# Optimization experiments

Hardware: AMD Instinct MI355X
Metric: run time of the kernel (lower is better)

## Reference

```python
import jax, jax.numpy as jnp
import numpy as np


def _gcn_conv(x, src, dst, W, b, n):
    """PyG-style GCNConv: symmetric-normalized aggregation with self-loops.
    out = D^{-1/2} (A + I) D^{-1/2} X W + b, deg computed with self-loops.
    """
    xw = x @ W  # [n, out]
    ones = jnp.ones(src.shape[0], dtype=x.dtype)
    deg = jax.ops.segment_sum(ones, dst, num_segments=n) + 1.0  # +1 self-loop
    dinv = jax.lax.rsqrt(deg)
    coef = dinv[src] * dinv[dst]  # [E]
    msg = xw[src] * coef[:, None]  # [E, out] gather + scale
    agg = jax.ops.segment_sum(msg, dst, num_segments=n)
    agg = agg + xw * (dinv * dinv)[:, None]  # self-loop term, norm = 1/deg
    return agg + b


def setup_inputs() -> dict:
    key = jax.random.key(0)
    ks = jax.random.split(key, 7)
    N, E = 500000, 8000000
    x = jax.random.normal(ks[0], (N, 2), dtype=jnp.float32)
    y1 = jax.random.normal(ks[1], (N,), dtype=jnp.float32)
    edge_index = jax.random.randint(ks[2], (2, E), 0, N, dtype=jnp.int64)
    s = 0.2
    W1 = jax.random.normal(ks[3], (3, 29), dtype=jnp.float32) * s
    b1 = jnp.zeros((29,), dtype=jnp.float32)
    W2 = jax.random.normal(ks[4], (32, 29), dtype=jnp.float32) * s
    b2 = jnp.zeros((29,), dtype=jnp.float32)
    W3 = jax.random.normal(ks[5], (32, 1), dtype=jnp.float32) * s
    b3 = jnp.zeros((1,), dtype=jnp.float32)
    return {"x": x, "y1": y1, "edge_index": edge_index,
            "W1": W1, "b1": b1, "W2": W2, "b2": b2, "W3": W3, "b3": b3}


def reference(x, y1, edge_index, W1, b1, W2, b2, W3, b3):
    n = x.shape[0]
    src, dst = edge_index[0], edge_index[1]
    inp = jnp.concatenate([x, y1[:, None]], axis=1)  # [N, 3]
    h = jax.nn.relu(_gcn_conv(inp, src, dst, W1, b1, n))  # [N, 29]
    h = jnp.concatenate([h, inp], axis=1)  # [N, 32] skip
    h = jax.nn.relu(_gcn_conv(h, src, dst, W2, b2, n))  # [N, 29]
    h = jnp.concatenate([h, inp], axis=1)  # [N, 32] skip
    h = _gcn_conv(h, src, dst, W3, b3, n)  # [N, 1]
    return h.reshape(-1)
```

## Files before the change

kernel.cpp:

```cpp
#include <hip/hip_runtime.h>
#include <hip/hip_fp16.h>


#define CAPB       17920
#define BSH2       10
#define BN2        1024
#define PACK_SHIFT 19
#define PACK_MASK  0x7FFFFu
#define SPLIT_CH   8192
#define DEST_CAP   17408

typedef int v4i __attribute__((ext_vector_type(4)));

__global__ __launch_bounds__(512) void split_kernel(
    const int* __restrict__ src, const int* __restrict__ dst,
    unsigned int* __restrict__ gcur, unsigned int* __restrict__ ebuf, int E) {
    __shared__ unsigned int hist[512];
    __shared__ unsigned int delta[512];
    __shared__ unsigned int wsum[8];
    __shared__ unsigned int tots;
    __shared__ unsigned int staged[SPLIT_CH];
    __shared__ unsigned short bid[SPLIT_CH];
    int tid = threadIdx.x;
    long long base = (long long)blockIdx.x * SPLIT_CH;
    hist[tid] = 0;
    __syncthreads();
    unsigned int s[16], d[16];
    if (base + SPLIT_CH <= E) {
        const v4i* s4 = (const v4i*)(src + base);
        const v4i* d4 = (const v4i*)(dst + base);
#pragma unroll
        for (int i = 0; i < 4; i++) {
            v4i sv = __builtin_nontemporal_load(s4 + tid + 512 * i);
            v4i dv = __builtin_nontemporal_load(d4 + tid + 512 * i);
            s[4 * i + 0] = (unsigned int)sv.x; d[4 * i + 0] = (unsigned int)dv.x;
            s[4 * i + 1] = (unsigned int)sv.y; d[4 * i + 1] = (unsigned int)dv.y;
            s[4 * i + 2] = (unsigned int)sv.z; d[4 * i + 2] = (unsigned int)dv.z;
            s[4 * i + 3] = (unsigned int)sv.w; d[4 * i + 3] = (unsigned int)dv.w;
        }
#pragma unroll
        for (int i = 0; i < 16; i++) atomicAdd(&hist[d[i] >> BSH2], 1u);
    } else {
#pragma unroll
        for (int i = 0; i < 16; i++) {
            long long e = base + tid + 512 * i;
            bool ok = e < E;
            s[i] = ok ? (unsigned int)src[e] : 0u;
            d[i] = ok ? (unsigned int)dst[e] : 0xFFFFFFFFu;
            if (ok) atomicAdd(&hist[d[i] >> BSH2], 1u);
        }
    }
    __syncthreads();
    unsigned int c = hist[tid];
    unsigned int v = c;
#pragma unroll
    for (int off = 1; off < 64; off <<= 1) {
        unsigned int t = __shfl_up(v, off, 64);
        if ((tid & 63) >= off) v += t;
    }
    int wv = tid >> 6;
    if ((tid & 63) == 63) wsum[wv] = v;
    __syncthreads();
    if (tid == 0) {
        unsigned int r = 0;
#pragma unroll
        for (int i = 0; i < 8; i++) { unsigned int t = wsum[i]; wsum[i] = r; r += t; }
        tots = r;
    }
    __syncthreads();
    unsigned int excl = v + wsum[wv] - c;
    unsigned int gb = c ? atomicAdd(&gcur[tid], c) : 0u;
    delta[tid] = gb - excl;
    hist[tid] = excl;
    __syncthreads();
#pragma unroll
    for (int i = 0; i < 16; i++) {
        if (d[i] != 0xFFFFFFFFu) {
            unsigned int bb = d[i] >> BSH2;
            unsigned int pos = atomicAdd(&hist[bb], 1u);
            staged[pos] = s[i] | ((d[i] & (BN2 - 1)) << PACK_SHIFT);
            bid[pos] = (unsigned short)bb;
        }
    }
    __syncthreads();
    unsigned int tot = tots;
    for (unsigned int i = tid; i < tot; i += 512) {
        unsigned int bb = bid[i];
        unsigned int rel = delta[bb] + i;
        if (rel < CAPB) ebuf[(size_t)bb * CAPB + rel] = staged[i];
    }
}

__global__ __launch_bounds__(1024) void build1_kernel(
    const unsigned int* __restrict__ gcur, const unsigned int* __restrict__ ebuf,
    const float* __restrict__ x, const float* __restrict__ y1,
    unsigned int* __restrict__ rowdeg, float4* __restrict__ u0,
    uint2* __restrict__ u0h, int N) {
    __shared__ unsigned int hist[BN2];
    __shared__ unsigned int wsum[16];
    int b = blockIdx.x, tid = threadIdx.x;
    hist[tid] = 0;
    unsigned int T = gcur[b]; if (T > CAPB) T = CAPB;
    const unsigned int* seg = ebuf + (size_t)b * CAPB;
    __syncthreads();
    for (unsigned int f = tid; f < T; f += 1024)
        atomicAdd(&hist[seg[f] >> PACK_SHIFT], 1u);
    __syncthreads();
    unsigned int cnt = hist[tid];
    unsigned int v = cnt;
#pragma unroll
    for (int off = 1; off < 64; off <<= 1) {
        unsigned int t = __shfl_up(v, off, 64);
        if ((tid & 63) >= off) v += t;
    }
    int wv = tid >> 6;
    if ((tid & 63) == 63) wsum[wv] = v;
    __syncthreads();
    if (tid == 0) {
        unsigned int r = 0;
#pragma unroll
        for (int i = 0; i < 16; i++) { unsigned int t = wsum[i]; wsum[i] = r; r += t; }
    }
    __syncthreads();
    unsigned int base = v + wsum[wv] - cnt;
    int n = (b << BSH2) + tid;
    if (n < N) {
        rowdeg[n] = base | (cnt << 16);
        float di = rsqrtf((float)cnt + 1.0f);
        float v0 = x[2 * n] * di, v1 = x[2 * n + 1] * di, v2 = y1[n] * di;
        u0[n] = make_float4(v0, v1, v2, di);
        union { __half2 h2[2]; uint2 u; } pk;
        pk.h2[0] = __floats2half2_rn(v0, v1);
        pk.h2[1] = __floats2half2_rn(v2, 0.f);
        u0h[n] = pk.u;
    }
}

__device__ __forceinline__ unsigned int sfetch2(const unsigned int* dest,
                                                const unsigned int* seg2,
                                                unsigned int j) {
    return (j < DEST_CAP) ? dest[j] : seg2[j];
}

__device__ __forceinline__ void walk_node(
    int gn, int q, unsigned int o, unsigned int e,
    const unsigned int* __restrict__ dest, const unsigned int* __restrict__ seg2,
    const uint2* __restrict__ u0h, const float4* __restrict__ u0,
    const float* __restrict__ W1, const float* __restrict__ b1,
    uint4* __restrict__ h1s) {
    unsigned int cnt = e - o;
    unsigned int hcnt = cnt >> 1;
    unsigned int j0 = o + (q ? hcnt : 0), j1 = q ? e : o + hcnt;
    float4 u = u0[gn];
    float sx = q ? 0.f : u.x, sy = q ? 0.f : u.y, sz = q ? 0.f : u.z;
    unsigned int j = j0;
    for (; j + 4 <= j1; j += 4) {
        unsigned int i0 = sfetch2(dest, seg2, j);
        unsigned int i1 = sfetch2(dest, seg2, j + 1);
        unsigned int i2 = sfetch2(dest, seg2, j + 2);
        unsigned int i3 = sfetch2(dest, seg2, j + 3);
        union { uint2 u; __half2 h[2]; } g0, g1, g2, g3;
        g0.u = u0h[i0]; g1.u = u0h[i1]; g2.u = u0h[i2]; g3.u = u0h[i3];
        float2 a0 = __half22float2(g0.h[0]), c0 = __half22float2(g0.h[1]);
        float2 a1 = __half22float2(g1.h[0]), c1 = __half22float2(g1.h[1]);
        float2 a2 = __half22float2(g2.h[0]), c2 = __half22float2(g2.h[1]);
        float2 a3 = __half22float2(g3.h[0]), c3 = __half22float2(g3.h[1]);
        sx += (a0.x + a1.x) + (a2.x + a3.x);
        sy += (a0.y + a1.y) + (a2.y + a3.y);
        sz += (c0.x + c1.x) + (c2.x + c3.x);
    }
    for (; j < j1; j++) {
        union { uint2 u; __half2 h[2]; } g;
        g.u = u0h[sfetch2(dest, seg2, j)];
        float2 a = __half22float2(g.h[0]);
        sx += a.x; sy += a.y; sz += __half2float(g.h[1].x);
    }
    sx += __shfl_xor(sx, 1, 64);
    sy += __shfl_xor(sy, 1, 64);
    sz += __shfl_xor(sz, 1, 64);
    float di = u.w;
    float a0 = sx * di, a1 = sy * di, a2 = sz * di;
    float hv[16];
#pragma unroll
    for (int i = 0; i < 16; i++) {
        int k = 16 * q + i;
        if (k < 29) {
            float vv = fmaf(a0, W1[k], fmaf(a1, W1[29 + k], fmaf(a2, W1[58 + k], b1[k])));
            hv[i] = fmaxf(vv, 0.0f) * di;
        } else {
            hv[i] = (k == 29) ? a0 : (k == 30) ? a1 : a2;
        }
    }
    union { __half2 h2[8]; uint4 u4[2]; } pk;
#pragma unroll
    for (int i = 0; i < 8; i++) pk.h2[i] = __floats2half2_rn(hv[2 * i], hv[2 * i + 1]);
    uint4* row = h1s + (size_t)gn * 4 + 2 * q;
    row[0] = pk.u4[0];
    row[1] = pk.u4[1];
}

__global__ __launch_bounds__(1024) void build2_kernel(
    const unsigned int* __restrict__ gcur, const unsigned int* __restrict__ ebuf,
    const unsigned int* __restrict__ rowdeg, const float4* __restrict__ u0,
    const uint2* __restrict__ u0h,
    const float* __restrict__ W1, const float* __restrict__ b1,
    unsigned int* __restrict__ ebuf2, uint4* __restrict__ h1s, int N) {
    __shared__ unsigned int cur[BN2];
    __shared__ unsigned int base2[BN2 + 1];
    __shared__ unsigned int dest[DEST_CAP];
    int b = blockIdx.x, tid = threadIdx.x;
    int gn0 = (b << BSH2);
    int n = gn0 + tid;
    unsigned int T = gcur[b]; if (T > CAPB) T = CAPB;
    unsigned int off = (n < N) ? (rowdeg[n] & 0xFFFFu) : T;
    cur[tid] = off; base2[tid] = off;
    if (tid == 0) base2[BN2] = T;
    const unsigned int* seg = ebuf + (size_t)b * CAPB;
    unsigned int* seg2 = ebuf2 + (size_t)b * CAPB;
    __syncthreads();
    for (unsigned int f = tid; f < T; f += 1024) {
        unsigned int p = seg[f];
        unsigned int dloc = p >> PACK_SHIFT;
        unsigned int pos = atomicAdd(&cur[dloc], 1u);
        unsigned int s = p & PACK_MASK;
        if (pos < DEST_CAP) dest[pos] = s;
        else                seg2[pos] = s;
    }
    __syncthreads();
    unsigned int m = T < DEST_CAP ? T : DEST_CAP;
    for (unsigned int i = tid; i < m; i += 1024) seg2[i] = dest[i];
    int q = tid & 1;
    int l0 = tid >> 1;
    int gnA = gn0 + l0;
    if (gnA < N)
        walk_node(gnA, q, base2[l0], base2[l0 + 1], dest, seg2, u0h, u0, W1, b1, h1s);
    int l1 = l0 + 512;
    int gnB = gn0 + l1;
    if (gnB < N)
        walk_node(gnB, q, base2[l1], base2[l1 + 1], dest, seg2, u0h, u0, W1, b1, h1s);
}

__device__ __forceinline__ void unpack8(float4 r, float* o) {
    union { float4 f; __half2 h[4]; } u; u.f = r;
    float2 a = __half22float2(u.h[0]); o[0] = a.x; o[1] = a.y;
    float2 b = __half22float2(u.h[1]); o[2] = b.x; o[3] = b.y;
    float2 c = __half22float2(u.h[2]); o[4] = c.x; o[5] = c.y;
    float2 d = __half22float2(u.h[3]); o[6] = d.x; o[7] = d.y;
}

__global__ __launch_bounds__(256) void pull2_kernel(
    const float4* __restrict__ h1f4, const unsigned int* __restrict__ rowdeg,
    const unsigned int* __restrict__ ebuf2, const float4* __restrict__ u0,
    const float* __restrict__ x, const float* __restrict__ y1,
    const float* __restrict__ W2, const float* __restrict__ b2,
    const float* __restrict__ W3, const float* __restrict__ b3,
    __half* __restrict__ zs, float* __restrict__ out, int N) {
    __shared__ float W2l[32 * 29];
    for (int i = threadIdx.x; i < 32 * 29; i += 256) W2l[i] = W2[i];
    int t = blockIdx.x * 256 + threadIdx.x;
    int n = t >> 2, q = t & 3;
    __syncthreads();
    if (n >= N) return;
    unsigned int rd = rowdeg[n];
    const unsigned int* lst = ebuf2 + (size_t)(n >> BSH2) * CAPB + (rd & 0xFFFFu);
    unsigned int cnt = rd >> 16;
    float acc[8] = {0.f, 0.f, 0.f, 0.f, 0.f, 0.f, 0.f, 0.f};
    unsigned int j = 0;
    for (; j + 4 <= cnt; j += 4) {
        unsigned int s0 = lst[j], s1 = lst[j + 1], s2 = lst[j + 2], s3 = lst[j + 3];
        float4 r0 = h1f4[(size_t)s0 * 4 + q];
        float4 r1 = h1f4[(size_t)s1 * 4 + q];
        float4 r2 = h1f4[(size_t)s2 * 4 + q];
        float4 r3 = h1f4[(size_t)s3 * 4 + q];
        float f0[8], f1[8], f2[8], f3[8];
        unpack8(r0, f0); unpack8(r1, f1); unpack8(r2, f2); unpack8(r3, f3);
#pragma unroll
        for (int i = 0; i < 8; i++) acc[i] += (f0[i] + f1[i]) + (f2[i] + f3[i]);
    }
    for (; j < cnt; j++) {
        float4 r0 = h1f4[(size_t)lst[j] * 4 + q];
        float f0[8]; unpack8(r0, f0);
#pragma unroll
        for (int i = 0; i < 8; i++) acc[i] += f0[i];
    }
    float hs[8];
    { float4 rs = h1f4[(size_t)n * 4 + q]; unpack8(rs, hs); }
    float di = u0[n].w;
    float g[8];
#pragma unroll
    for (int i = 0; i < 8; i++) {
        int jj = 8 * q + i;
        g[i] = (jj < 29) ? (acc[i] + hs[i]) * di
                         : hs[i];
    }
    float p29[29];
#pragma unroll
    for (int kk = 0; kk < 29; kk++) p29[kk] = 0.f;
#pragma unroll
    for (int i = 0; i < 8; i++) {
        float gi = g[i];
        const float* wr = &W2l[(8 * q + i) * 29];
#pragma unroll
        for (int kk = 0; kk < 29; kk++) p29[kk] = fmaf(gi, wr[kk], p29[kk]);
    }
#pragma unroll
    for (int kk = 0; kk < 29; kk++) {
        p29[kk] += __shfl_xor(p29[kk], 1, 64);
        p29[kk] += __shfl_xor(p29[kk], 2, 64);
    }
    if (q == 0) {
        float z = 0.0f;
#pragma unroll
        for (int kk = 0; kk < 29; kk++)
            z = fmaf(fmaxf(p29[kk] + b2[kk], 0.0f), W3[kk], z);
        z = fmaf(x[2 * n], W3[29], z);
        z = fmaf(x[2 * n + 1], W3[30], z);
        z = fmaf(y1[n], W3[31], z);
        zs[n]  = __float2half_rn(z * di);
        out[n] = fmaf(z * di, di, b3[0]);
    }
}

__global__ void pull3_kernel(const __half* __restrict__ zs, const float4* __restrict__ u0,
                             const unsigned int* __restrict__ rowdeg,
                             const unsigned int* __restrict__ ebuf2,
                             float* __restrict__ out, int N) {
    int n = blockIdx.x * blockDim.x + threadIdx.x;
    if (n >= N) return;
    unsigned int rd = rowdeg[n];
    const unsigned int* lst = ebuf2 + (size_t)(n >> BSH2) * CAPB + (rd & 0xFFFFu);
    unsigned int cnt = rd >> 16;
    float s = 0.f;
    unsigned int j = 0;
    for (; j + 4 <= cnt; j += 4) {
        unsigned int i0 = __builtin_nontemporal_load(lst + j);
        unsigned int i1 = __builtin_nontemporal_load(lst + j + 1);
        unsigned int i2 = __builtin_nontemporal_load(lst + j + 2);
        unsigned int i3 = __builtin_nontemporal_load(lst + j + 3);
        s += (__half2float(zs[i0]) + __half2float(zs[i1]))
           + (__half2float(zs[i2]) + __half2float(zs[i3]));
    }
    for (; j < cnt; j++) s += __half2float(zs[lst[j]]);
    out[n] += s * u0[n].w;
}

extern "C" void kernel_launch(void* const* d_in, const int* in_sizes, int n_in,
                              void* d_out, int out_size, void* d_ws, size_t ws_size,
                              hipStream_t stream) {
    const float* x  = (const float*)d_in[0];
    const float* y1 = (const float*)d_in[1];
    const int*   ei = (const int*)d_in[2];
    const float* W1 = (const float*)d_in[3];
    const float* b1 = (const float*)d_in[4];
    const float* W2 = (const float*)d_in[5];
    const float* b2 = (const float*)d_in[6];
    const float* W3 = (const float*)d_in[7];
    const float* b3 = (const float*)d_in[8];
    float* out = (float*)d_out;

    int N = in_sizes[1];
    int E = in_sizes[2] / 2;
    const int* src = ei;
    const int* dst = ei + E;

    size_t Ns = (size_t)N;
    int nb = (N + BN2 - 1) >> BSH2;
    size_t segtot = (size_t)512 * CAPB;

    float* ws = (float*)d_ws;
    float4*       u0     = (float4*)ws;
    __half*       zs     = (__half*)(ws + 4 * Ns);
    unsigned int* rowdeg = (unsigned int*)(ws + 5 * Ns);
    uint2*        u0h    = (uint2*)(ws + 6 * Ns);
    unsigned int* gcur   = (unsigned int*)(ws + 8 * Ns);
    unsigned int* ebuf   = gcur + 512;
    unsigned int* ebuf2  = ebuf + segtot;
    uint4*        h1s    = (uint4*)(ebuf2 + segtot);

    hipMemsetAsync(gcur, 0, 512 * sizeof(unsigned int), stream);

    const int gS = (E + SPLIT_CH - 1) / SPLIT_CH;
    const int gN = (N + 255) / 256;
    const int g4 = (4 * N + 255) / 256;
    split_kernel <<<gS, 512, 0, stream>>>(src, dst, gcur, ebuf, E);
    build1_kernel<<<nb, 1024, 0, stream>>>(gcur, ebuf, x, y1, rowdeg, u0, u0h, N);
    build2_kernel<<<nb, 1024, 0, stream>>>(gcur, ebuf, rowdeg, u0, u0h, W1, b1,
                                           ebuf2, h1s, N);
    pull2_kernel <<<g4, 256, 0, stream>>>((const float4*)h1s, rowdeg, ebuf2, u0,
                                          x, y1, W2, b2, W3, b3, zs, out, N);
    pull3_kernel <<<gN, 256, 0, stream>>>(zs, u0, rowdeg, ebuf2, out, N);
}
```

Baseline: 431.3 us.

## Compute degrees via global atomics in split, fold CSR offsets into build2

Degree counting moves into split_kernel as global atomics on a per-node array, and a lightweight prep_kernel computes normalized features from it. This removes build1's separate pass over the bucketed edge buffer. build2 now builds the local histogram and prefix sum itself, writes rowdeg, then scatters. Several loads and stores become nontemporal. The cost is 8M extra global atomics, one more memset, and a second read of each segment inside build2.

New measurement: 729.3 us. +69.1%, slower.

```diff
diff --git a/kernel.cpp b/kernel.cpp
--- a/kernel.cpp
+++ b/kernel.cpp
@@ -11,10 +11,13 @@
 #define DEST_CAP   17408
 
 typedef int v4i __attribute__((ext_vector_type(4)));
+typedef float v4f __attribute__((ext_vector_type(4)));
+typedef unsigned int v4u __attribute__((ext_vector_type(4)));
 
 __global__ __launch_bounds__(512) void split_kernel(
     const int* __restrict__ src, const int* __restrict__ dst,
-    unsigned int* __restrict__ gcur, unsigned int* __restrict__ ebuf, int E) {
+    unsigned int* __restrict__ gcur, unsigned int* __restrict__ deg,
+    unsigned int* __restrict__ ebuf, int E) {
     __shared__ unsigned int hist[512];
     __shared__ unsigned int delta[512];
     __shared__ unsigned int wsum[8];
@@ -40,6 +43,8 @@
         }
 #pragma unroll
         for (int i = 0; i < 16; i++) atomicAdd(&hist[d[i] >> BSH2], 1u);
+#pragma unroll
+        for (int i = 0; i < 16; i++) atomicAdd(&deg[d[i]], 1u);
     } else {
 #pragma unroll
         for (int i = 0; i < 16; i++) {
@@ -47,7 +52,7 @@
             bool ok = e < E;
             s[i] = ok ? (unsigned int)src[e] : 0u;
             d[i] = ok ? (unsigned int)dst[e] : 0xFFFFFFFFu;
-            if (ok) atomicAdd(&hist[d[i] >> BSH2], 1u);
+            if (ok) { atomicAdd(&hist[d[i] >> BSH2], 1u); atomicAdd(&deg[d[i]], 1u); }
         }
     }
     __syncthreads();
@@ -87,53 +92,26 @@
     for (unsigned int i = tid; i < tot; i += 512) {
         unsigned int bb = bid[i];
         unsigned int rel = delta[bb] + i;
-        if (rel < CAPB) ebuf[(size_t)bb * CAPB + rel] = staged[i];
-    }
-}
-
-__global__ __launch_bounds__(1024) void build1_kernel(
-    const unsigned int* __restrict__ gcur, const unsigned int* __restrict__ ebuf,
-    const float* __restrict__ x, const float* __restrict__ y1,
-    unsigned int* __restrict__ rowdeg, float4* __restrict__ u0,
+        if (rel < CAPB)
+            __builtin_nontemporal_store(staged[i], &ebuf[(size_t)bb * CAPB + rel]);
+    }
+}
+
+__global__ __launch_bounds__(256) void prep_kernel(
+    const unsigned int* __restrict__ deg, const float* __restrict__ x,
+    const float* __restrict__ y1, float4* __restrict__ u0,
     uint2* __restrict__ u0h, int N) {
-    __shared__ unsigned int hist[BN2];
-    __shared__ unsigned int wsum[16];
-    int b = blockIdx.x, tid = threadIdx.x;
-    hist[tid] = 0;
-    unsigned int T = gcur[b]; if (T > CAPB) T = CAPB;
-    const unsigned int* seg = ebuf + (size_t)b * CAPB;
-    __syncthreads();
-    for (unsigned int f = tid; f < T; f += 1024)
-        atomicAdd(&hist[seg[f] >> PACK_SHIFT], 1u);
-    __syncthreads();
-    unsigned int cnt = hist[tid];
-    unsigned int v = cnt;
-#pragma unroll
-    for (int off = 1; off < 64; off <<= 1) {
-        unsigned int t = __shfl_up(v, off, 64);
-        if ((tid & 63) >= off) v += t;
-    }
-    int wv = tid >> 6;
-    if ((tid & 63) == 63) wsum[wv] = v;
-    __syncthreads();
-    if (tid == 0) {
-        unsigned int r = 0;
-#pragma unroll
-        for (int i = 0; i < 16; i++) { unsigned int t = wsum[i]; wsum[i] = r; r += t; }
-    }
-    __syncthreads();
-    unsigned int base = v + wsum[wv] - cnt;
-    int n = (b << BSH2) + tid;
-    if (n < N) {
-        rowdeg[n] = base | (cnt << 16);
-        float di = rsqrtf((float)cnt + 1.0f);
-        float v0 = x[2 * n] * di, v1 = x[2 * n + 1] * di, v2 = y1[n] * di;
-        u0[n] = make_float4(v0, v1, v2, di);
-        union { __half2 h2[2]; uint2 u; } pk;
-        pk.h2[0] = __floats2half2_rn(v0, v1);
-        pk.h2[1] = __floats2half2_rn(v2, 0.f);
-        u0h[n] = pk.u;
-    }
+    int n = blockIdx.x * 256 + threadIdx.x;
+    if (n >= N) return;
+    unsigned int cnt = deg[n];
+    float di = rsqrtf((float)cnt + 1.0f);
+    float2 xv = ((const float2*)x)[n];
+    float v0 = xv.x * di, v1 = xv.y * di, v2 = y1[n] * di;
+    u0[n] = make_float4(v0, v1, v2, di);
+    union { __half2 h2[2]; uint2 u; } pk;
+    pk.h2[0] = __floats2half2_rn(v0, v1);
+    pk.h2[1] = __floats2half2_rn(v2, 0.f);
+    u0h[n] = pk.u;
 }
 
 __device__ __forceinline__ unsigned int sfetch2(const unsigned int* dest,
@@ -151,7 +129,7 @@
     unsigned int cnt = e - o;
     unsigned int hcnt = cnt >> 1;
     unsigned int j0 = o + (q ? hcnt : 0), j1 = q ? e : o + hcnt;
-    float4 u = u0[gn];
+    v4f u = __builtin_nontemporal_load((const v4f*)&u0[gn]);
     float sx = q ? 0.f : u.x, sy = q ? 0.f : u.y, sz = q ? 0.f : u.z;
     unsigned int j = j0;
     for (; j + 4 <= j1; j += 4) {
@@ -191,35 +169,58 @@
             hv[i] = (k == 29) ? a0 : (k == 30) ? a1 : a2;
         }
     }
-    union { __half2 h2[8]; uint4 u4[2]; } pk;
+    union { __half2 h2[8]; v4u u4[2]; } pk;
 #pragma unroll
     for (int i = 0; i < 8; i++) pk.h2[i] = __floats2half2_rn(hv[2 * i], hv[2 * i + 1]);
-    uint4* row = h1s + (size_t)gn * 4 + 2 * q;
-    row[0] = pk.u4[0];
-    row[1] = pk.u4[1];
+    v4u* row = (v4u*)(h1s + (size_t)gn * 4 + 2 * q);
+    __builtin_nontemporal_store(pk.u4[0], row);
+    __builtin_nontemporal_store(pk.u4[1], row + 1);
 }
 
 __global__ __launch_bounds__(1024) void build2_kernel(
     const unsigned int* __restrict__ gcur, const unsigned int* __restrict__ ebuf,
-    const unsigned int* __restrict__ rowdeg, const float4* __restrict__ u0,
-    const uint2* __restrict__ u0h,
+    const float4* __restrict__ u0, const uint2* __restrict__ u0h,
     const float* __restrict__ W1, const float* __restrict__ b1,
+    unsigned int* __restrict__ rowdeg,
     unsigned int* __restrict__ ebuf2, uint4* __restrict__ h1s, int N) {
     __shared__ unsigned int cur[BN2];
     __shared__ unsigned int base2[BN2 + 1];
+    __shared__ unsigned int wsum[16];
     __shared__ unsigned int dest[DEST_CAP];
     int b = blockIdx.x, tid = threadIdx.x;
     int gn0 = (b << BSH2);
     int n = gn0 + tid;
     unsigned int T = gcur[b]; if (T > CAPB) T = CAPB;
-    unsigned int off = (n < N) ? (rowdeg[n] & 0xFFFFu) : T;
-    cur[tid] = off; base2[tid] = off;
-    if (tid == 0) base2[BN2] = T;
     const unsigned int* seg = ebuf + (size_t)b * CAPB;
     unsigned int* seg2 = ebuf2 + (size_t)b * CAPB;
+    cur[tid] = 0;
+    __syncthreads();
+    for (unsigned int f = tid; f < T; f += 1024)
+        atomicAdd(&cur[__builtin_nontemporal_load(seg + f) >> PACK_SHIFT], 1u);
+    __syncthreads();
+    unsigned int cnt = cur[tid];
+    unsigned int v = cnt;
+#pragma unroll
+    for (int off = 1; off < 64; off <<= 1) {
+        unsigned int t = __shfl_up(v, off, 64);
+        if ((tid & 63) >= off) v += t;
+    }
+    int wv = tid >> 6;
+    if ((tid & 63) == 63) wsum[wv] = v;
+    __syncthreads();
+    if (tid == 0) {
+        unsigned int r = 0;
+#pragma unroll
+        for (int i = 0; i < 16; i++) { unsigned int t = wsum[i]; wsum[i] = r; r += t; }
+    }
+    __syncthreads();
+    unsigned int base = v + wsum[wv] - cnt;
+    if (n < N) __builtin_nontemporal_store(base | (cnt << 16), &rowdeg[n]);
+    cur[tid] = base; base2[tid] = base;
+    if (tid == 0) base2[BN2] = T;
     __syncthreads();
     for (unsigned int f = tid; f < T; f += 1024) {
-        unsigned int p = seg[f];
+        unsigned int p = __builtin_nontemporal_load(seg + f);
         unsigned int dloc = p >> PACK_SHIFT;
         unsigned int pos = atomicAdd(&cur[dloc], 1u);
         unsigned int s = p & PACK_MASK;
@@ -228,7 +229,8 @@
     }
     __syncthreads();
     unsigned int m = T < DEST_CAP ? T : DEST_CAP;
-    for (unsigned int i = tid; i < m; i += 1024) seg2[i] = dest[i];
+    for (unsigned int i = tid; i < m; i += 1024)
+        __builtin_nontemporal_store(dest[i], &seg2[i]);
     int q = tid & 1;
     int l0 = tid >> 1;
     int gnA = gn0 + l0;
@@ -373,19 +375,20 @@
     unsigned int* rowdeg = (unsigned int*)(ws + 5 * Ns);
     uint2*        u0h    = (uint2*)(ws + 6 * Ns);
     unsigned int* gcur   = (unsigned int*)(ws + 8 * Ns);
-    unsigned int* ebuf   = gcur + 512;
+    unsigned int* deg    = gcur + 512;
+    unsigned int* ebuf   = deg + Ns;
     unsigned int* ebuf2  = ebuf + segtot;
     uint4*        h1s    = (uint4*)(ebuf2 + segtot);
 
-    hipMemsetAsync(gcur, 0, 512 * sizeof(unsigned int), stream);
+    hipMemsetAsync(gcur, 0, (512 + Ns) * sizeof(unsigned int), stream);
 
     const int gS = (E + SPLIT_CH - 1) / SPLIT_CH;
     const int gN = (N + 255) / 256;
     const int g4 = (4 * N + 255) / 256;
-    split_kernel <<<gS, 512, 0, stream>>>(src, dst, gcur, ebuf, E);
-    build1_kernel<<<nb, 1024, 0, stream>>>(gcur, ebuf, x, y1, rowdeg, u0, u0h, N);
-    build2_kernel<<<nb, 1024, 0, stream>>>(gcur, ebuf, rowdeg, u0, u0h, W1, b1,
-                                           ebuf2, h1s, N);
+    split_kernel <<<gS, 512, 0, stream>>>(src, dst, gcur, deg, ebuf, E);
+    prep_kernel  <<<gN, 256, 0, stream>>>(deg, x, y1, u0, u0h, N);
+    build2_kernel<<<nb, 1024, 0, stream>>>(gcur, ebuf, u0, u0h, W1, b1,
+                                           rowdeg, ebuf2, h1s, N);
     pull2_kernel <<<g4, 256, 0, stream>>>((const float4*)h1s, rowdeg, ebuf2, u0,
                                           x, y1, W2, b2, W3, b3, zs, out, N);
     pull3_kernel <<<gN, 256, 0, stream>>>(zs, u0, rowdeg, ebuf2, out, N);
```
